# Kernel tuning notes

Measured on AMD Instinct MI355X. Metric: run time of the kernel, lower is better.

## Reference

```python
import jax, jax.numpy as jnp
import numpy as np


def setup_inputs() -> dict:
    key = jax.random.key(0)
    B, S, D = 64, 1024, 1024
    ks = jax.random.split(key, 13)
    bound = 1.0 / np.sqrt(D)
    u = lambda k, shape: jax.random.uniform(k, shape, jnp.float32, -bound, bound)
    inp = {
        "emb": jax.random.normal(ks[0], (B, S, D), jnp.float32),
        "W_ii": u(ks[1], (D, D)), "b_ii": u(ks[2], (D,)),
        "W_if": u(ks[3], (D, D)), "b_if": u(ks[4], (D,)),
        "W_ig": u(ks[5], (D, D)), "b_ig": u(ks[6], (D,)),
        "W_io": u(ks[7], (D, D)), "b_io": u(ks[8], (D,)),
        "W_hi": u(ks[9], (D, D)),
        "W_hf": u(ks[10], (D, D)),
        "W_hg": u(ks[11], (D, D)),
        "W_ho": u(ks[12], (D, D)),
    }
    return inp


def _lstm_forward(emb, W_ii, b_ii, W_if, b_if, W_ig, b_ig, W_io, b_io,
                  W_hi, W_hf, W_hg, W_ho):
    B, S, D = emb.shape
    # Precompute all input projections in one batched GEMM: [B,S,4D]
    Wx = jnp.concatenate([W_ii, W_if, W_ig, W_io], axis=0)      # [4D, D]
    bx = jnp.concatenate([b_ii, b_if, b_ig, b_io], axis=0)      # [4D]
    x_proj = jnp.einsum('bsd,ed->bse', emb, Wx) + bx            # [B,S,4D]
    x_proj = jnp.swapaxes(x_proj, 0, 1)                         # [S,B,4D]
    # Fuse the 4 hidden matmuls into one [D,4D] weight
    Wh = jnp.concatenate([W_hi, W_hf, W_hg, W_ho], axis=0)      # [4D, D]

    h0 = jnp.zeros((B, D), emb.dtype)
    c0 = jnp.zeros((B, D), emb.dtype)

    def step(carry, xp_t):
        h, c = carry
        gates = xp_t + h @ Wh.T                                 # [B,4D]
        xi, xf, xg, xo = jnp.split(gates, 4, axis=-1)
        i_t = jax.nn.sigmoid(xi)
        f_t = jax.nn.sigmoid(xf)
        g_t = jnp.tanh(xg)
        o_t = jax.nn.sigmoid(xo)
        c = f_t * c + i_t * g_t
        h = o_t * jnp.tanh(c)
        return (h, c), None

    (h, c), _ = jax.lax.scan(step, (h0, c0), x_proj)
    return h


def reference(emb, W_ii, b_ii, W_if, b_if, W_ig, b_ig, W_io, b_io,
              W_hi, W_hf, W_hg, W_ho):
    return _lstm_forward(emb, W_ii, b_ii, W_if, b_if, W_ig, b_ig,
                         W_io, b_io, W_hi, W_hf, W_hg, W_ho)
```

## Files before the change

### kernel.cpp

```cpp
#include <hip/hip_runtime.h>
#include <stdint.h>

#define NB 64
#define NS 1024
#define ND 1024
#define NG 4096
#define CHUNK 128
#define NCHUNK 8
#define RING 32

typedef __attribute__((ext_vector_type(4))) float f32x4;
typedef __attribute__((ext_vector_type(8))) short bf16x8;

__device__ __forceinline__ float bf2f(uint16_t u) {
  return __uint_as_float(((uint32_t)u) << 16);
}
__device__ __forceinline__ uint16_t f2bf(float f) {
  uint32_t x = __float_as_uint(f);
  return (uint16_t)((x + 0x7fffu + ((x >> 16) & 1u)) >> 16);
}
__device__ __forceinline__ float sigmoidf_(float x) {
  return 1.f / (1.f + __expf(-x));
}
__device__ __forceinline__ float tanhf_(float x) {
  return 1.f - 2.f / (__expf(x + x) + 1.f);
}
__device__ __forceinline__ void gload_lds16(const void* g, void* l) {
  __builtin_amdgcn_global_load_lds(
      (const __attribute__((address_space(1))) uint32_t*)g,
      (__attribute__((address_space(3))) uint32_t*)l, 16, 0, 0);
}
__device__ __forceinline__ void gload_lds16_nc(const void* g, void* l) {
  __builtin_amdgcn_global_load_lds(
      (const __attribute__((address_space(1))) uint32_t*)g,
      (__attribute__((address_space(3))) uint32_t*)l, 16, 0, 17);
}

__global__ void k_cvt(const float* __restrict__ src, uint16_t* __restrict__ dst, int n4) {
  int stride = gridDim.x * blockDim.x;
  for (int i = blockIdx.x * blockDim.x + threadIdx.x; i < n4; i += stride) {
    float4 v = ((const float4*)src)[i];
    ushort4 o;
    o.x = f2bf(v.x); o.y = f2bf(v.y); o.z = f2bf(v.z); o.w = f2bf(v.w);
    ((ushort4*)dst)[i] = o;
  }
}

__global__ void k_cvt8(const float* w0, const float* w1, const float* w2, const float* w3,
                       const float* w4, const float* w5, const float* w6, const float* w7,
                       uint16_t* wx, uint16_t* wh) {
  int which = blockIdx.x >> 8;
  const float* src;
  uint16_t* dst;
  if      (which == 0) { src = w0; dst = wx; }
  else if (which == 1) { src = w1; dst = wx + 1048576; }
  else if (which == 2) { src = w2; dst = wx + 2097152; }
  else if (which == 3) { src = w3; dst = wx + 3145728; }
  else if (which == 4) { src = w4; dst = wh; }
  else if (which == 5) { src = w5; dst = wh + 1048576; }
  else if (which == 6) { src = w6; dst = wh + 2097152; }
  else                 { src = w7; dst = wh + 3145728; }
  for (int i = (blockIdx.x & 255) * 256 + threadIdx.x; i < 262144; i += 65536) {
    float4 v = ((const float4*)src)[i];
    ushort4 o;
    o.x = f2bf(v.x); o.y = f2bf(v.y); o.z = f2bf(v.z); o.w = f2bf(v.w);
    ((ushort4*)dst)[i] = o;
  }
}

__device__ __forceinline__ void gemm_tile(const uint16_t* __restrict__ A0,
                                          const uint16_t* __restrict__ Wx,
                                          uint16_t* __restrict__ XP,
                                          int b, int nb, int tid, char* lmem) {
  uint16_t* lAx = (uint16_t*)lmem;
  uint16_t* lBx = (uint16_t*)(lmem + 8192);
  const uint16_t* B0 = Wx + (size_t)(nb * 128) * ND;
  const int lane = tid & 63, wv = tid >> 6;
  const int m_off = (wv >> 1) << 6, n_off = (wv & 1) << 6;

  f32x4 acc[4][4] = {};
  for (int kb = 0; kb < ND / 32; ++kb) {
    const int k0 = kb * 32;
#pragma unroll
    for (int j = 0; j < 2; ++j) {
      int cid = j * 256 + tid;
      int row = cid >> 2, cc = cid & 3;
      int cs = cc ^ (row & 3);
      gload_lds16(A0 + (size_t)row * ND + k0 + cs * 8, (char*)lAx + cid * 16);
      gload_lds16(B0 + (size_t)row * ND + k0 + cs * 8, (char*)lBx + cid * 16);
    }
    __syncthreads();
    bf16x8 af[4], bfr[4];
#pragma unroll
    for (int i = 0; i < 4; ++i) {
      int row = m_off + i * 16 + (lane & 15);
      int ch = (lane >> 4) ^ (row & 3);
      af[i] = *(const bf16x8*)((const char*)lAx + row * 64 + ch * 16);
      int rowb = n_off + i * 16 + (lane & 15);
      int chb = (lane >> 4) ^ (rowb & 3);
      bfr[i] = *(const bf16x8*)((const char*)lBx + rowb * 64 + chb * 16);
    }
#pragma unroll
    for (int i = 0; i < 4; ++i)
#pragma unroll
      for (int j2 = 0; j2 < 4; ++j2)
        acc[i][j2] = __builtin_amdgcn_mfma_f32_16x16x32_bf16(af[i], bfr[j2], acc[i][j2], 0, 0, 0);
    __syncthreads();
  }
#pragma unroll
  for (int i = 0; i < 4; ++i)
#pragma unroll
    for (int j2 = 0; j2 < 4; ++j2)
#pragma unroll
      for (int r = 0; r < 4; ++r) {
        int m = m_off + i * 16 + ((lane >> 4) << 2) + r;
        int n = nb * 128 + n_off + j2 * 16 + (lane & 15);
        XP[((size_t)(m * NB + b)) * NG + n] = f2bf(acc[i][j2][r]);
      }
}

__global__ __launch_bounds__(512, 2) void k_fused(
    const uint16_t* __restrict__ embb,
    const uint16_t* __restrict__ Wx,
    const uint16_t* __restrict__ Wh,
    uint16_t* __restrict__ xpA, uint16_t* __restrict__ xpB,
    const float* __restrict__ b_i, const float* __restrict__ b_f,
    const float* __restrict__ b_g, const float* __restrict__ b_o,
    uint16_t* __restrict__ hring,
    float* __restrict__ cbuf,
    uint32_t* __restrict__ flags,
    float* __restrict__ out, int chunk) {
  extern __shared__ char smem[];
  const int bid = blockIdx.x;
  const int tid = threadIdx.x;

  if (chunk < 0 || bid >= 128) {
    const int gc = (chunk < 0) ? 0 : chunk + 1;
    if (gc >= NCHUNK) return;
    uint16_t* XP = (gc & 1) ? xpB : xpA;
    const int nw = (chunk < 0) ? 512 : 256;
    const int widx = ((chunk < 0) ? bid : bid - 128) * 2 + (tid >> 8);
    const int t256 = tid & 255;
    char* lmem = smem + ((tid >> 8) << 14);
    const int t0g = gc * CHUNK;
    for (int job = widx; job < 64 * 32; job += nw) {
      int b = job & 63, nb = job >> 6;
      gemm_tile(embb + ((size_t)b * NS + t0g) * ND, Wx, XP, b, nb, t256, lmem);
    }
    return;
  }

  uint16_t* lH = (uint16_t*)smem;
  int* lds_sync = (int*)(smem + 32768);
  const int t0 = chunk * CHUNK;
  const uint16_t* XP = (chunk & 1) ? xpB : xpA;

  const int lane = tid & 63, wv = tid >> 6;
  const int xcd = bid & 7;
  const int g_b = xcd >> 1;
  const int g_d = (xcd & 1) + ((bid >> 3) << 1);

  const int q = lane >> 4, nl = lane & 15;
  const int g = nl & 3;
  const int d_loc = wv * 4 + (nl >> 2);
  const int dg = g_d * 32 + d_loc;
  const int bg0 = g_b * 16 + q * 4;

  const uint16_t* wrow = Wh + ((size_t)g * ND + dg) * ND;
  bf16x8 wfr[32];
#pragma unroll
  for (int kk = 0; kk < 32; ++kk)
    wfr[kk] = *(const bf16x8*)(wrow + kk * 32 + q * 8);

  const float* bptr = (g == 0) ? b_i : (g == 1) ? b_f : (g == 2) ? b_g : b_o;
  const float Bv = bptr[dg];

  float c0, c1, c2, c3;
  if (t0 == 0) {
    c0 = c1 = c2 = c3 = 0.f;
  } else {
    c0 = cbuf[(size_t)(bg0 + 0) * ND + dg];
    c1 = cbuf[(size_t)(bg0 + 1) * ND + dg];
    c2 = cbuf[(size_t)(bg0 + 2) * ND + dg];
    c3 = cbuf[(size_t)(bg0 + 3) * ND + dg];
  }

  if (tid == 0)
    __hip_atomic_store(lds_sync, t0, __ATOMIC_RELAXED, __HIP_MEMORY_SCOPE_WORKGROUP);
  __syncthreads();

  const uint16_t* xp0 = XP + ((size_t)bg0) * NG + ((size_t)g << 10) + dg;
  uint16_t xc0 = xp0[0], xc1 = xp0[NG], xc2 = xp0[2 * (size_t)NG], xc3 = xp0[3 * (size_t)NG];

#pragma unroll 1
  for (int t = t0; t < t0 + CHUNK; ++t) {
    f32x4 a0 = {0,0,0,0}, a1 = {0,0,0,0}, a2 = {0,0,0,0}, a3 = {0,0,0,0};
    if (t > 0) {
      if (wv == 0) {
        const uint32_t* fl = flags + ((((size_t)(t - 1) * 4 + g_b) << 5) + (lane & 31)) * 4;
        uint32_t v;
        do {
          v = __hip_atomic_load(fl, __ATOMIC_RELAXED, __HIP_MEMORY_SCOPE_AGENT);
        } while (__any(v == 0));
        if (lane == 0)
          __hip_atomic_store(lds_sync, t, __ATOMIC_RELAXED, __HIP_MEMORY_SCOPE_WORKGROUP);
      } else {
        while (__hip_atomic_load(lds_sync, __ATOMIC_RELAXED, __HIP_MEMORY_SCOPE_WORKGROUP) < t) {}
      }
      const uint16_t* hbase = hring + (size_t)((t - 1) & (RING - 1)) * NB * ND;
#pragma unroll
      for (int j = 0; j < 4; ++j) {
        int ch = wv * 64 + j * 512 + lane;
        int row = ch >> 7, c = ch & 127;
        const uint16_t* src = hbase + (size_t)(g_b * 16 + row) * ND + ((c ^ (row & 7)) << 3);
        gload_lds16_nc(src, (char*)lH + ch * 16);
      }
      __syncthreads();
    }

    int tn = t + 1 < t0 + CHUNK ? t + 1 : t;
    const uint16_t* xpn = XP + (((size_t)(tn - t0) * NB) + bg0) * NG + ((size_t)g << 10) + dg;
    uint16_t xn0 = xpn[0], xn1 = xpn[NG], xn2 = xpn[2 * (size_t)NG], xn3 = xpn[3 * (size_t)NG];

    if (t > 0) {
#pragma unroll
      for (int kk = 0; kk < 32; ++kk) {
        int cs = (kk * 4 + q) ^ (nl & 7);
        bf16x8 af = *(const bf16x8*)((const char*)lH + nl * 2048 + cs * 16);
        if ((kk & 3) == 0)      a0 = __builtin_amdgcn_mfma_f32_16x16x32_bf16(af, wfr[kk], a0, 0, 0, 0);
        else if ((kk & 3) == 1) a1 = __builtin_amdgcn_mfma_f32_16x16x32_bf16(af, wfr[kk], a1, 0, 0, 0);
        else if ((kk & 3) == 2) a2 = __builtin_amdgcn_mfma_f32_16x16x32_bf16(af, wfr[kk], a2, 0, 0, 0);
        else                    a3 = __builtin_amdgcn_mfma_f32_16x16x32_bf16(af, wfr[kk], a3, 0, 0, 0);
      }
    }

    float xr[4] = { bf2f(xc0), bf2f(xc1), bf2f(xc2), bf2f(xc3) };
    float cc[4] = { c0, c1, c2, c3 };
    float hval = 0.f;
#pragma unroll
    for (int r = 0; r < 4; ++r) {
      float v = a0[r] + a1[r] + a2[r] + a3[r] + xr[r] + Bv;
      float act = (g == 2) ? tanhf_(v) : sigmoidf_(v);
      float s1 = __shfl_xor(act, 1);
      float pe = (g & 1) ? s1 : act;
      float po = (g & 1) ? act : s1;
      float qe = __shfl_xor(pe, 2);
      float qo = __shfl_xor(po, 2);
      float gi = (g & 2) ? qe : pe;
      float gf = (g & 2) ? qo : po;
      float gg2 = (g & 2) ? pe : qe;
      float go = (g & 2) ? po : qo;
      float cn = __builtin_fmaf(gf, cc[r], gi * gg2);
      cc[r] = cn;
      float h = go * tanhf_(cn);
      if (r == g) hval = h;
    }
    c0 = cc[0]; c1 = cc[1]; c2 = cc[2]; c3 = cc[3];

    {
      int hv = (int)f2bf(hval);
      int p = __shfl_xor(hv, 4);
      uint32_t v32 = ((nl >> 2) & 1) ? ((uint32_t)p | ((uint32_t)hv << 16))
                                     : ((uint32_t)hv | ((uint32_t)p << 16));
      uint32_t hi = (uint32_t)__shfl_xor((int)v32, 8);
      if (nl < 4) {
        uint64_t val = (uint64_t)v32 | ((uint64_t)hi << 32);
        uint16_t* dst = hring + (size_t)(t & (RING - 1)) * NB * ND
                        + (size_t)(g_b * 16 + q * 4 + nl) * ND + g_d * 32 + wv * 4;
        __hip_atomic_store((uint64_t*)dst, val, __ATOMIC_RELAXED, __HIP_MEMORY_SCOPE_AGENT);
      }
    }
    if (t == NS - 1) out[(size_t)(bg0 + g) * ND + dg] = hval;

    __syncthreads();
    if (tid == 0)
      __hip_atomic_store(flags + ((((size_t)t * 4 + g_b) << 5) + g_d) * 4, 1u,
                         __ATOMIC_RELAXED, __HIP_MEMORY_SCOPE_AGENT);

    xc0 = xn0; xc1 = xn1; xc2 = xn2; xc3 = xn3;
  }

  float cstore = (g == 0) ? c0 : (g == 1) ? c1 : (g == 2) ? c2 : c3;
  cbuf[(size_t)(bg0 + g) * ND + dg] = cstore;
}

extern "C" void kernel_launch(void* const* d_in, const int* in_sizes, int n_in,
                              void* d_out, int out_size, void* d_ws, size_t ws_size,
                              hipStream_t stream) {
  const float* emb = (const float*)d_in[0];
  const float* W_ii = (const float*)d_in[1];
  const float* b_ii = (const float*)d_in[2];
  const float* W_if = (const float*)d_in[3];
  const float* b_if = (const float*)d_in[4];
  const float* W_ig = (const float*)d_in[5];
  const float* b_ig = (const float*)d_in[6];
  const float* W_io = (const float*)d_in[7];
  const float* b_io = (const float*)d_in[8];
  const float* W_hi = (const float*)d_in[9];
  const float* W_hf = (const float*)d_in[10];
  const float* W_hg = (const float*)d_in[11];
  const float* W_ho = (const float*)d_in[12];

  char* ws = (char*)d_ws;
  uint16_t* embb  = (uint16_t*)ws;
  uint16_t* wx    = (uint16_t*)(ws + 134217728);
  uint16_t* wh    = (uint16_t*)(ws + 142606336);
  uint16_t* xpA   = (uint16_t*)(ws + 150994944);
  uint16_t* xpB   = (uint16_t*)(ws + 218103808);
  uint16_t* hring = (uint16_t*)(ws + 285212672);
  float*    cbuf  = (float*)(ws + 289406976);
  uint32_t* flags = (uint32_t*)(ws + 289669120);

  hipMemsetAsync(flags, 0, 2097152, stream);

  k_cvt<<<2048, 256, 0, stream>>>(emb, embb, 64 * 1024 * 1024 / 4);
  k_cvt8<<<2048, 256, 0, stream>>>(W_ii, W_if, W_ig, W_io, W_hi, W_hf, W_hg, W_ho, wx, wh);

  const int SHM = 98304;
  hipFuncSetAttribute((const void*)k_fused, hipFuncAttributeMaxDynamicSharedMemorySize, SHM);

  k_fused<<<256, 512, SHM, stream>>>(embb, wx, wh, xpA, xpB, b_ii, b_if, b_ig, b_io,
                                     hring, cbuf, flags, (float*)d_out, -1);
  for (int chk = 0; chk < NCHUNK; ++chk)
    k_fused<<<256, 512, SHM, stream>>>(embb, wx, wh, xpA, xpB, b_ii, b_if, b_ig, b_io,
                                       hring, cbuf, flags, (float*)d_out, chk);
}
```

Before: 3.597 ms.

## Split hidden-GEMM K across wave pairs, each computing two output tiles

Each wave now covers half of the K dimension for two adjacent hidden-unit tiles instead of all of K for one tile. Each LDS A-fragment read therefore feeds two MFMAs, which halves the per-step LDS reads of h. The wave pairs swap their partial sums through a new LDS scratch area and an extra __syncthreads each timestep. That barrier and the LDS exchange add latency to the serial recurrence, and the new scratch region needs enough shared memory allocated. The final cell-state store also writes the same values more than once.

```diff
diff --git a/kernel.cpp b/kernel.cpp
--- a/kernel.cpp
+++ b/kernel.cpp
@@ -152,6 +152,7 @@
 
   uint16_t* lH = (uint16_t*)smem;
   int* lds_sync = (int*)(smem + 32768);
+  float* shr = (float*)(smem + 32832);
   const int t0 = chunk * CHUNK;
   const uint16_t* XP = (chunk & 1) ? xpB : xpA;
 
@@ -162,27 +163,37 @@
 
   const int q = lane >> 4, nl = lane & 15;
   const int g = nl & 3;
-  const int d_loc = wv * 4 + (nl >> 2);
+  const int cp = wv & 3;
+  const int kh = wv >> 2;
+  const int Tf = (cp << 1) | kh;
+  const int d_loc = Tf * 4 + (nl >> 2);
   const int dg = g_d * 32 + d_loc;
+  const int dg0 = g_d * 32 + (cp << 3) + (nl >> 2);
+  const int dg1 = dg0 + 4;
   const int bg0 = g_b * 16 + q * 4;
 
-  const uint16_t* wrow = Wh + ((size_t)g * ND + dg) * ND;
-  bf16x8 wfr[32];
-#pragma unroll
-  for (int kk = 0; kk < 32; ++kk)
-    wfr[kk] = *(const bf16x8*)(wrow + kk * 32 + q * 8);
+  bf16x8 wfr0[16], wfr1[16];
+  {
+    const uint16_t* w0 = Wh + ((size_t)g * ND + dg0) * ND + kh * 512;
+    const uint16_t* w1 = Wh + ((size_t)g * ND + dg1) * ND + kh * 512;
+#pragma unroll
+    for (int kk = 0; kk < 16; ++kk) {
+      wfr0[kk] = *(const bf16x8*)(w0 + kk * 32 + q * 8);
+      wfr1[kk] = *(const bf16x8*)(w1 + kk * 32 + q * 8);
+    }
+  }
 
   const float* bptr = (g == 0) ? b_i : (g == 1) ? b_f : (g == 2) ? b_g : b_o;
   const float Bv = bptr[dg];
 
-  float c0, c1, c2, c3;
+  float c0, c1, c2s, c3;
   if (t0 == 0) {
-    c0 = c1 = c2 = c3 = 0.f;
+    c0 = c1 = c2s = c3 = 0.f;
   } else {
-    c0 = cbuf[(size_t)(bg0 + 0) * ND + dg];
-    c1 = cbuf[(size_t)(bg0 + 1) * ND + dg];
-    c2 = cbuf[(size_t)(bg0 + 2) * ND + dg];
-    c3 = cbuf[(size_t)(bg0 + 3) * ND + dg];
+    c0  = cbuf[(size_t)(bg0 + 0) * ND + dg];
+    c1  = cbuf[(size_t)(bg0 + 1) * ND + dg];
+    c2s = cbuf[(size_t)(bg0 + 2) * ND + dg];
+    c3  = cbuf[(size_t)(bg0 + 3) * ND + dg];
   }
 
   if (tid == 0)
@@ -194,7 +205,7 @@
 
 #pragma unroll 1
   for (int t = t0; t < t0 + CHUNK; ++t) {
-    f32x4 a0 = {0,0,0,0}, a1 = {0,0,0,0}, a2 = {0,0,0,0}, a3 = {0,0,0,0};
+    f32x4 a0 = {0,0,0,0}, a1 = {0,0,0,0}, e0 = {0,0,0,0}, e1 = {0,0,0,0};
     if (t > 0) {
       if (wv == 0) {
         const uint32_t* fl = flags + ((((size_t)(t - 1) * 4 + g_b) << 5) + (lane & 31)) * 4;
@@ -224,22 +235,34 @@
 
     if (t > 0) {
 #pragma unroll
-      for (int kk = 0; kk < 32; ++kk) {
-        int cs = (kk * 4 + q) ^ (nl & 7);
+      for (int kk = 0; kk < 16; ++kk) {
+        int kg = (kh << 4) + kk;
+        int cs = (kg * 4 + q) ^ (nl & 7);
         bf16x8 af = *(const bf16x8*)((const char*)lH + nl * 2048 + cs * 16);
-        if ((kk & 3) == 0)      a0 = __builtin_amdgcn_mfma_f32_16x16x32_bf16(af, wfr[kk], a0, 0, 0, 0);
-        else if ((kk & 3) == 1) a1 = __builtin_amdgcn_mfma_f32_16x16x32_bf16(af, wfr[kk], a1, 0, 0, 0);
-        else if ((kk & 3) == 2) a2 = __builtin_amdgcn_mfma_f32_16x16x32_bf16(af, wfr[kk], a2, 0, 0, 0);
-        else                    a3 = __builtin_amdgcn_mfma_f32_16x16x32_bf16(af, wfr[kk], a3, 0, 0, 0);
-      }
-    }
+        if (kk & 1) {
+          a1 = __builtin_amdgcn_mfma_f32_16x16x32_bf16(af, wfr0[kk], a1, 0, 0, 0);
+          e1 = __builtin_amdgcn_mfma_f32_16x16x32_bf16(af, wfr1[kk], e1, 0, 0, 0);
+        } else {
+          a0 = __builtin_amdgcn_mfma_f32_16x16x32_bf16(af, wfr0[kk], a0, 0, 0, 0);
+          e0 = __builtin_amdgcn_mfma_f32_16x16x32_bf16(af, wfr1[kk], e0, 0, 0, 0);
+        }
+      }
+    }
+
+    f32x4 p0 = a0 + a1;
+    f32x4 p1 = e0 + e1;
+    f32x4 pk = kh ? p1 : p0;
+    f32x4 ps = kh ? p0 : p1;
+    *(f32x4*)(shr + ((wv ^ 4) << 8) + (lane << 2)) = ps;
+    __syncthreads();
+    pk += *(const f32x4*)(shr + (wv << 8) + (lane << 2));
 
     float xr[4] = { bf2f(xc0), bf2f(xc1), bf2f(xc2), bf2f(xc3) };
-    float cc[4] = { c0, c1, c2, c3 };
+    float cc[4] = { c0, c1, c2s, c3 };
     float hval = 0.f;
 #pragma unroll
     for (int r = 0; r < 4; ++r) {
-      float v = a0[r] + a1[r] + a2[r] + a3[r] + xr[r] + Bv;
+      float v = pk[r] + xr[r] + Bv;
       float act = (g == 2) ? tanhf_(v) : sigmoidf_(v);
       float s1 = __shfl_xor(act, 1);
       float pe = (g & 1) ? s1 : act;
@@ -255,7 +278,7 @@
       float h = go * tanhf_(cn);
       if (r == g) hval = h;
     }
-    c0 = cc[0]; c1 = cc[1]; c2 = cc[2]; c3 = cc[3];
+    c0 = cc[0]; c1 = cc[1]; c2s = cc[2]; c3 = cc[3];
 
     {
       int hv = (int)f2bf(hval);
@@ -266,7 +289,7 @@
       if (nl < 4) {
         uint64_t val = (uint64_t)v32 | ((uint64_t)hi << 32);
         uint16_t* dst = hring + (size_t)(t & (RING - 1)) * NB * ND
-                        + (size_t)(g_b * 16 + q * 4 + nl) * ND + g_d * 32 + wv * 4;
+                        + (size_t)(g_b * 16 + q * 4 + nl) * ND + g_d * 32 + Tf * 4;
         __hip_atomic_store((uint64_t*)dst, val, __ATOMIC_RELAXED, __HIP_MEMORY_SCOPE_AGENT);
       }
     }
@@ -280,8 +303,14 @@
     xc0 = xn0; xc1 = xn1; xc2 = xn2; xc3 = xn3;
   }
 
-  float cstore = (g == 0) ? c0 : (g == 1) ? c1 : (g == 2) ? c2 : c3;
-  cbuf[(size_t)(bg0 + g) * ND + dg] = cstore;
+  cbuf[(size_t)(bg0 + 0) * ND + dg] = c0;
+  if (g == 1) cbuf[(size_t)(bg0 + 1) * ND + dg] = c1;
+  if (g == 2) cbuf[(size_t)(bg0 + 2) * ND + dg] = c2s;
+  if (g == 3) cbuf[(size_t)(bg0 + 3) * ND + dg] = c3;
+  {
+    float cstore = (g == 0) ? c0 : (g == 1) ? c1 : (g == 2) ? c2s : c3;
+    cbuf[(size_t)(bg0 + g) * ND + dg] = cstore;
+  }
 }
 
 extern "C" void kernel_launch(void* const* d_in, const int* in_sizes, int n_in,
```

Result: faster. 3.413 ms (-5.1%).
